# Kernel optimization log

Measured on AMD Instinct MI355X. Metric: run time of the kernel, lower is better.

## Reference

```python
import jax, jax.numpy as jnp
import numpy as np


def setup_inputs() -> dict:
    key = jax.random.key(0)
    k1, k2, k3, k4, k5 = jax.random.split(key, 5)
    N, M, K = 200000, 50, 4
    T = 1000.0
    ti = jnp.sort(jax.random.uniform(k1, (N,), dtype=jnp.float32) * T)
    mi = jax.random.randint(k2, (N,), 0, M, dtype=jnp.int64)
    mu_at_events = jax.random.uniform(k3, (N,), dtype=jnp.float32) * 0.5 + 0.05
    alpha = jax.random.uniform(k4, (K, M, M), dtype=jnp.float32) * 0.1
    gamma = jax.random.uniform(k5, (K,), dtype=jnp.float32) * 2.0 + 0.5
    return {"ti": ti, "mi": mi, "mu_at_events": mu_at_events, "alpha": alpha, "gamma": gamma}


def _hawkes_logsum(ti, mi, mu_at_events, alpha, gamma):
    # ti: [N] sorted event times; mi: [N] event types in [0, M)
    # alpha: [K, M, M]; gamma: [K]; mu_at_events: [N]
    N = ti.shape[0]
    M = alpha.shape[1]
    # inter-event gaps; dt[0] = 0 so the first event has zero excitation state
    dt = jnp.concatenate([jnp.zeros((1,), ti.dtype), ti[1:] - ti[:-1]])  # [N]
    a = jnp.exp(-gamma[None, :] * dt[:, None])  # [N, K] decay factors
    # one-hot of the PREVIOUS event's type (row 0 is all-zero, matching e_mi)
    prev_onehot = jnp.zeros((N, M), ti.dtype).at[jnp.arange(1, N), mi[:-1]].set(1.0)
    b = a[:, None, :] * prev_onehot[:, :, None]  # [N, M, K]

    # linear recurrence S_i = a_i * S_{i-1} + b_i via associative scan
    # combine((a1,b1),(a2,b2)) = (a1*a2, a2*b1 + b2)
    def combine(x, y):
        a1, b1 = x
        a2, b2 = y
        return (a1 * a2, a2[:, None, :] * b1 + b2)

    _, S = jax.lax.associative_scan(combine, (a, b))  # S: [N, M, K]
    # S[i, m, k] = sum_{j < i, m_j = m} exp(-gamma_k (t_i - t_j))
    alpha_at = alpha[:, mi, :]  # [K, N, M] rows of alpha for each event's type
    lam = mu_at_events + jnp.einsum('knm,nmk,k->n', alpha_at, S, gamma)  # [N]
    return jnp.sum(jnp.log(lam))


def reference(ti, mi, mu_at_events, alpha, gamma):
    return _hawkes_logsum(ti, mi, mu_at_events, alpha, gamma)
```

## Files before the change

kernel.cpp:

```cpp
#include <hip/hip_runtime.h>
#include <hip/hip_bf16.h>

#define CHUNK 256
#define MM 50
#define KK 4
#define STATE (MM*KK)
#define ASTRIDE 51
#define SUP 32
#define NSMAX 26

__device__ __forceinline__ unsigned short f2bf(float x) {
  unsigned u = __float_as_uint(x);
  u += 0x7fffu + ((u >> 16) & 1u);
  return (unsigned short)(u >> 16);
}

__global__ __launch_bounds__(256) void phase1(
    const float* __restrict__ ti, const int* __restrict__ mi,
    const float* __restrict__ gamma, float* __restrict__ chunkB,
    float* __restrict__ out0, int N, int G) {
  int g = blockIdx.x, tid = threadIdx.x;
  if (g == 0 && tid == 0) out0[0] = 0.f;
  int l = g * CHUNK;
  int r = min(N, l + CHUNK);
  __shared__ float Bs[STATE];
  __shared__ float g4[KK];
  if (tid < STATE) Bs[tid] = 0.f;
  if (tid < KK) g4[tid] = gamma[tid];
  __syncthreads();
  float t_end = ti[r - 1];
  int j0 = (g == 0) ? 0 : (l - 1);
  int j = j0 + tid;
  if (j <= r - 2) {
    int m = mi[j];
    float dt = t_end - ti[j];
    #pragma unroll
    for (int k = 0; k < KK; ++k)
      atomicAdd(&Bs[m * KK + k], __expf(-g4[k] * dt));
  }
  __syncthreads();
  if (tid < STATE) chunkB[(size_t)g * STATE + tid] = Bs[tid];
}

__global__ __launch_bounds__(256) void phase2a(
    const float* __restrict__ ti, const float* __restrict__ gamma,
    const float* __restrict__ chunkB, float* __restrict__ localpref,
    float* __restrict__ superB, int N, int G) {
  int s = blockIdx.x, tid = threadIdx.x;
  int g0 = s * SUP;
  int gN = min(G, g0 + SUP) - g0;
  __shared__ float te[SUP + 1];
  if (tid <= SUP) {
    int gg = g0 + tid;
    te[tid] = (gg == 0) ? ti[0] : ti[min(N, gg * CHUNK) - 1];
  }
  __syncthreads();
  if (tid >= STATE) return;
  float gk = gamma[tid & 3];
  float B[SUP];
  #pragma unroll
  for (int u = 0; u < SUP; ++u)
    B[u] = (u < gN) ? chunkB[(size_t)(g0 + u) * STATE + tid] : 0.f;
  float S = 0.f;
  #pragma unroll
  for (int u = 0; u < SUP; ++u) {
    if (u < gN) {
      localpref[(size_t)(g0 + u) * STATE + tid] = S;
      if (u == 0) {
        S = B[0];
      } else {
        float a = __expf(-gk * (te[u + 1] - te[u]));
        S = a * S + B[u];
      }
    }
  }
  superB[(size_t)s * STATE + tid] = S;
}

__global__ __launch_bounds__(256) void phase2b(
    const float* __restrict__ ti, const float* __restrict__ gamma,
    const float* __restrict__ superB, float* __restrict__ superpref,
    int N, int nS) {
  int tid = threadIdx.x;
  __shared__ float tlast[NSMAX];
  if (tid < NSMAX)
    tlast[tid] = ti[min(SUP * (tid + 1) * CHUNK, N) - 1];
  __syncthreads();
  if (tid >= STATE) return;
  float gk = gamma[tid & 3];
  float B[NSMAX];
  #pragma unroll
  for (int s = 0; s < NSMAX; ++s)
    B[s] = (s < nS) ? superB[(size_t)s * STATE + tid] : 0.f;
  float S = 0.f;
  superpref[tid] = 0.f;
  #pragma unroll
  for (int s = 0; s < NSMAX; ++s) {
    if (s < nS) {
      if (s == 0) S = B[0];
      else {
        float a = __expf(-gk * (tlast[s] - tlast[s - 1]));
        S = a * S + B[s];
      }
      if (s + 1 < nS) superpref[(size_t)(s + 1) * STATE + tid] = S;
    }
  }
}

__global__ __launch_bounds__(256) void phase3(
    const float* __restrict__ ti, const int* __restrict__ mi,
    const float* __restrict__ mu, const float* __restrict__ alpha,
    const float* __restrict__ gamma, const float* __restrict__ localpref,
    const float* __restrict__ superpref, float* __restrict__ out, int N, int G) {
  int g = blockIdx.x, tid = threadIdx.x;
  int l = g * CHUNK;
  int r = min(N, l + CHUNK);
  int cnt = r - l;
  int sup = g / SUP;

  __shared__ uint2  ALGh[MM * ASTRIDE];
  __shared__ float4 Fj[CHUNK];
  __shared__ int    cj[CHUNK];
  __shared__ float  Q[4][STATE];
  __shared__ float  red[256];

  float gk0 = gamma[0], gk1 = gamma[1], gk2 = gamma[2], gk3 = gamma[3];

  for (int i = tid; i < 4 * STATE; i += 256) ((float*)Q)[i] = 0.f;

  for (int e = tid; e < MM * MM; e += 256) {
    int c = e / MM, cp = e - c * MM;
    float a0 = gk0 * alpha[e];
    float a1 = gk1 * alpha[2500 + e];
    float a2 = gk2 * alpha[5000 + e];
    float a3 = gk3 * alpha[7500 + e];
    ALGh[c * ASTRIDE + cp] =
        make_uint2((unsigned)f2bf(a0) | ((unsigned)f2bf(a1) << 16),
                   (unsigned)f2bf(a2) | ((unsigned)f2bf(a3) << 16));
  }

  int j = l - 1 + tid;
  float t_ref = ti[(g == 0) ? 0 : (l - 1)];
  float4 myF = make_float4(0.f, 0.f, 0.f, 0.f);
  int myc = 0;
  bool valid = (j >= 0) && (j <= r - 2);
  if (valid) {
    myc = mi[j];
    float tj = ti[j] - t_ref;
    myF = make_float4(__expf(gk0 * tj), __expf(gk1 * tj),
                      __expf(gk2 * tj), __expf(gk3 * tj));
  }
  cj[tid] = myc;
  Fj[tid] = myF;
  __syncthreads();

  if (valid) {
    float* q = &Q[tid >> 6][myc * KK];
    atomicAdd(q + 0, myF.x); atomicAdd(q + 1, myF.y);
    atomicAdd(q + 2, myF.z); atomicAdd(q + 3, myF.w);
  }
  __syncthreads();

  if (tid < STATE) {
    float gk = gamma[tid & 3];
    float t_hi = (g > 0) ? ti[(size_t)g * CHUNK - 1] : ti[0];
    float t_lo = (sup > 0) ? ti[(size_t)sup * SUP * CHUNK - 1] : ti[0];
    float D = __expf(-gk * (t_hi - t_lo));
    float sin_v = localpref[(size_t)g * STATE + tid]
                + D * superpref[(size_t)sup * STATE + tid];
    float q0 = Q[0][tid], q1 = Q[1][tid], q2 = Q[2][tid];
    Q[0][tid] = sin_v;
    Q[1][tid] = sin_v + q0;
    Q[2][tid] = sin_v + q0 + q1;
    Q[3][tid] = sin_v + q0 + q1 + q2;
  }
  __syncthreads();

  float local = 0.f;
  if (tid < cnt) {
    int n = l + tid;
    int c_n = mi[n];
    const uint2* arow = &ALGh[c_n * ASTRIDE];
    const float4* wb = (const float4*)&Q[tid >> 6][0];
    float4 acc = make_float4(0.f, 0.f, 0.f, 0.f);
    #pragma unroll 2
    for (int m = 0; m < MM; ++m) {
      uint2 p = arow[m];
      float4 w = wb[m];
      acc.x += __uint_as_float(p.x << 16)          * w.x;
      acc.y += __uint_as_float(p.x & 0xffff0000u)  * w.y;
      acc.z += __uint_as_float(p.y << 16)          * w.z;
      acc.w += __uint_as_float(p.y & 0xffff0000u)  * w.w;
    }
    #pragma unroll 4
    for (int s = (tid & ~63); s <= tid; ++s) {
      uint2 p = arow[cj[s]];
      float4 f = Fj[s];
      acc.x += __uint_as_float(p.x << 16)          * f.x;
      acc.y += __uint_as_float(p.x & 0xffff0000u)  * f.y;
      acc.z += __uint_as_float(p.y << 16)          * f.z;
      acc.w += __uint_as_float(p.y & 0xffff0000u)  * f.w;
    }
    float tn = ti[n] - t_ref;
    float lam = mu[n]
              + __expf(-gk0 * tn) * acc.x + __expf(-gk1 * tn) * acc.y
              + __expf(-gk2 * tn) * acc.z + __expf(-gk3 * tn) * acc.w;
    local = __logf(lam);
  }
  red[tid] = local;
  __syncthreads();
  for (int off = 128; off > 0; off >>= 1) {
    if (tid < off) red[tid] += red[tid + off];
    __syncthreads();
  }
  if (tid == 0) atomicAdd(out, red[0]);
}

extern "C" void kernel_launch(void* const* d_in, const int* in_sizes, int n_in,
                              void* d_out, int out_size, void* d_ws, size_t ws_size,
                              hipStream_t stream) {
  const float* ti    = (const float*)d_in[0];
  const int*   mi    = (const int*)d_in[1];
  const float* mu    = (const float*)d_in[2];
  const float* alpha = (const float*)d_in[3];
  const float* gamma = (const float*)d_in[4];
  float* out = (float*)d_out;
  int N = in_sizes[0];
  int G = (N + CHUNK - 1) / CHUNK;
  int nS = (G + SUP - 1) / SUP;
  float* chunkB    = (float*)d_ws;
  float* localpref = chunkB + (size_t)G * STATE;
  float* superB    = localpref + (size_t)G * STATE;
  float* superpref = superB + (size_t)NSMAX * STATE;

  phase1<<<G, 256, 0, stream>>>(ti, mi, gamma, chunkB, out, N, G);
  phase2a<<<nS, 256, 0, stream>>>(ti, gamma, chunkB, localpref, superB, N, G);
  phase2b<<<1, 256, 0, stream>>>(ti, gamma, superB, superpref, N, nS);
  phase3<<<G, 256, 0, stream>>>(ti, mi, mu, alpha, gamma, localpref, superpref, out, N, G);
}
```

Baseline: 106.1 us.

## Fuse four scan phases into one cooperative kernel with grid syncs

Replaces the four separate launches with a single cooperative kernel that uses grid.sync between the chunk-sum, super-chunk scan, top-level scan and evaluation stages. Chunk sums are now derived from the phase-3 shared-memory partials, so the separate pass over the events is gone. The intra-chunk subgroup size drops from 64 to 32 (8 subgroups), which shortens the per-event quadratic loop. The packed alpha table is split into two 32-bit arrays. The cost is three grid-wide barriers and the constraint that all 782 blocks must be co-resident, which the __launch_bounds__(256,4) hint and the larger shared footprint have to allow.

Result: slower. 328.5 us (+209.5%).

```diff
diff --git a/kernel.cpp b/kernel.cpp
--- a/kernel.cpp
+++ b/kernel.cpp
@@ -1,5 +1,8 @@
 #include <hip/hip_runtime.h>
 #include <hip/hip_bf16.h>
+#include <hip/hip_cooperative_groups.h>
+
+namespace cg = cooperative_groups;
 
 #define CHUNK 256
 #define MM 50
@@ -8,6 +11,8 @@
 #define ASTRIDE 51
 #define SUP 32
 #define NSMAX 26
+#define NSUB 8
+#define SUBSZ 32
 
 __device__ __forceinline__ unsigned short f2bf(float x) {
   unsigned u = __float_as_uint(x);
@@ -15,118 +20,34 @@
   return (unsigned short)(u >> 16);
 }
 
-__global__ __launch_bounds__(256) void phase1(
-    const float* __restrict__ ti, const int* __restrict__ mi,
-    const float* __restrict__ gamma, float* __restrict__ chunkB,
-    float* __restrict__ out0, int N, int G) {
-  int g = blockIdx.x, tid = threadIdx.x;
-  if (g == 0 && tid == 0) out0[0] = 0.f;
-  int l = g * CHUNK;
-  int r = min(N, l + CHUNK);
-  __shared__ float Bs[STATE];
-  __shared__ float g4[KK];
-  if (tid < STATE) Bs[tid] = 0.f;
-  if (tid < KK) g4[tid] = gamma[tid];
-  __syncthreads();
-  float t_end = ti[r - 1];
-  int j0 = (g == 0) ? 0 : (l - 1);
-  int j = j0 + tid;
-  if (j <= r - 2) {
-    int m = mi[j];
-    float dt = t_end - ti[j];
-    #pragma unroll
-    for (int k = 0; k < KK; ++k)
-      atomicAdd(&Bs[m * KK + k], __expf(-g4[k] * dt));
-  }
-  __syncthreads();
-  if (tid < STATE) chunkB[(size_t)g * STATE + tid] = Bs[tid];
-}
-
-__global__ __launch_bounds__(256) void phase2a(
-    const float* __restrict__ ti, const float* __restrict__ gamma,
-    const float* __restrict__ chunkB, float* __restrict__ localpref,
-    float* __restrict__ superB, int N, int G) {
-  int s = blockIdx.x, tid = threadIdx.x;
-  int g0 = s * SUP;
-  int gN = min(G, g0 + SUP) - g0;
-  __shared__ float te[SUP + 1];
-  if (tid <= SUP) {
-    int gg = g0 + tid;
-    te[tid] = (gg == 0) ? ti[0] : ti[min(N, gg * CHUNK) - 1];
-  }
-  __syncthreads();
-  if (tid >= STATE) return;
-  float gk = gamma[tid & 3];
-  float B[SUP];
-  #pragma unroll
-  for (int u = 0; u < SUP; ++u)
-    B[u] = (u < gN) ? chunkB[(size_t)(g0 + u) * STATE + tid] : 0.f;
-  float S = 0.f;
-  #pragma unroll
-  for (int u = 0; u < SUP; ++u) {
-    if (u < gN) {
-      localpref[(size_t)(g0 + u) * STATE + tid] = S;
-      if (u == 0) {
-        S = B[0];
-      } else {
-        float a = __expf(-gk * (te[u + 1] - te[u]));
-        S = a * S + B[u];
-      }
-    }
-  }
-  superB[(size_t)s * STATE + tid] = S;
-}
-
-__global__ __launch_bounds__(256) void phase2b(
-    const float* __restrict__ ti, const float* __restrict__ gamma,
-    const float* __restrict__ superB, float* __restrict__ superpref,
-    int N, int nS) {
-  int tid = threadIdx.x;
-  __shared__ float tlast[NSMAX];
-  if (tid < NSMAX)
-    tlast[tid] = ti[min(SUP * (tid + 1) * CHUNK, N) - 1];
-  __syncthreads();
-  if (tid >= STATE) return;
-  float gk = gamma[tid & 3];
-  float B[NSMAX];
-  #pragma unroll
-  for (int s = 0; s < NSMAX; ++s)
-    B[s] = (s < nS) ? superB[(size_t)s * STATE + tid] : 0.f;
-  float S = 0.f;
-  superpref[tid] = 0.f;
-  #pragma unroll
-  for (int s = 0; s < NSMAX; ++s) {
-    if (s < nS) {
-      if (s == 0) S = B[0];
-      else {
-        float a = __expf(-gk * (tlast[s] - tlast[s - 1]));
-        S = a * S + B[s];
-      }
-      if (s + 1 < nS) superpref[(size_t)(s + 1) * STATE + tid] = S;
-    }
-  }
-}
-
-__global__ __launch_bounds__(256) void phase3(
+__global__ __launch_bounds__(256, 4) void hawkes_all(
     const float* __restrict__ ti, const int* __restrict__ mi,
     const float* __restrict__ mu, const float* __restrict__ alpha,
-    const float* __restrict__ gamma, const float* __restrict__ localpref,
-    const float* __restrict__ superpref, float* __restrict__ out, int N, int G) {
+    const float* __restrict__ gamma,
+    float* __restrict__ chunkB, float* __restrict__ localpref,
+    float* __restrict__ superB, float* __restrict__ superpref,
+    float* __restrict__ out, int N, int G, int nS) {
+  cg::grid_group grid = cg::this_grid();
   int g = blockIdx.x, tid = threadIdx.x;
   int l = g * CHUNK;
   int r = min(N, l + CHUNK);
   int cnt = r - l;
   int sup = g / SUP;
 
-  __shared__ uint2  ALGh[MM * ASTRIDE];
-  __shared__ float4 Fj[CHUNK];
-  __shared__ int    cj[CHUNK];
-  __shared__ float  Q[4][STATE];
-  __shared__ float  red[256];
+  __shared__ unsigned P0[MM * ASTRIDE];
+  __shared__ unsigned P1[MM * ASTRIDE];
+  __shared__ __align__(16) float4 Fj[CHUNK];
+  __shared__ int   cj[CHUNK];
+  __shared__ __align__(16) float Q[NSUB][STATE];
+  __shared__ float red[256];
+  __shared__ float te[SUP + 1];
+  __shared__ float tlast[NSMAX];
+
+  if (g == 0 && tid == 0) out[0] = 0.f;
 
   float gk0 = gamma[0], gk1 = gamma[1], gk2 = gamma[2], gk3 = gamma[3];
 
-  for (int i = tid; i < 4 * STATE; i += 256) ((float*)Q)[i] = 0.f;
+  for (int i = tid; i < NSUB * STATE; i += 256) ((float*)Q)[i] = 0.f;
 
   for (int e = tid; e < MM * MM; e += 256) {
     int c = e / MM, cp = e - c * MM;
@@ -134,9 +55,8 @@
     float a1 = gk1 * alpha[2500 + e];
     float a2 = gk2 * alpha[5000 + e];
     float a3 = gk3 * alpha[7500 + e];
-    ALGh[c * ASTRIDE + cp] =
-        make_uint2((unsigned)f2bf(a0) | ((unsigned)f2bf(a1) << 16),
-                   (unsigned)f2bf(a2) | ((unsigned)f2bf(a3) << 16));
+    P0[c * ASTRIDE + cp] = (unsigned)f2bf(a0) | ((unsigned)f2bf(a1) << 16);
+    P1[c * ASTRIDE + cp] = (unsigned)f2bf(a2) | ((unsigned)f2bf(a3) << 16);
   }
 
   int j = l - 1 + tid;
@@ -155,7 +75,7 @@
   __syncthreads();
 
   if (valid) {
-    float* q = &Q[tid >> 6][myc * KK];
+    float* q = &Q[tid >> 5][myc * KK];
     atomicAdd(q + 0, myF.x); atomicAdd(q + 1, myF.y);
     atomicAdd(q + 2, myF.z); atomicAdd(q + 3, myF.w);
   }
@@ -163,16 +83,88 @@
 
   if (tid < STATE) {
     float gk = gamma[tid & 3];
-    float t_hi = (g > 0) ? ti[(size_t)g * CHUNK - 1] : ti[0];
+    float t_end = ti[r - 1];
+    float Dend = __expf(-gk * (t_end - t_ref));
+    float btot = 0.f;
+    #pragma unroll
+    for (int q = 0; q < NSUB; ++q) btot += Q[q][tid];
+    chunkB[(size_t)g * STATE + tid] = Dend * btot;
+  }
+
+  grid.sync();
+
+  if (g < nS) {
+    int g0 = g * SUP;
+    int gN = min(G, g0 + SUP) - g0;
+    if (tid <= SUP) {
+      int gg = g0 + tid;
+      te[tid] = (gg == 0) ? ti[0] : ti[min(N, gg * CHUNK) - 1];
+    }
+    __syncthreads();
+    if (tid < STATE) {
+      float gk = gamma[tid & 3];
+      float B[SUP];
+      #pragma unroll
+      for (int u = 0; u < SUP; ++u)
+        B[u] = (u < gN) ? chunkB[(size_t)(g0 + u) * STATE + tid] : 0.f;
+      float S = 0.f;
+      #pragma unroll
+      for (int u = 0; u < SUP; ++u) {
+        if (u < gN) {
+          localpref[(size_t)(g0 + u) * STATE + tid] = S;
+          if (u == 0) S = B[0];
+          else {
+            float a = __expf(-gk * (te[u + 1] - te[u]));
+            S = a * S + B[u];
+          }
+        }
+      }
+      superB[(size_t)g * STATE + tid] = S;
+    }
+  }
+
+  grid.sync();
+
+  if (g == 0) {
+    if (tid < NSMAX)
+      tlast[tid] = ti[min(SUP * (tid + 1) * CHUNK, N) - 1];
+    __syncthreads();
+    if (tid < STATE) {
+      float gk = gamma[tid & 3];
+      float B[NSMAX];
+      #pragma unroll
+      for (int s = 0; s < NSMAX; ++s)
+        B[s] = (s < nS) ? superB[(size_t)s * STATE + tid] : 0.f;
+      float S = 0.f;
+      superpref[tid] = 0.f;
+      #pragma unroll
+      for (int s = 0; s < NSMAX; ++s) {
+        if (s < nS) {
+          if (s == 0) S = B[0];
+          else {
+            float a = __expf(-gk * (tlast[s] - tlast[s - 1]));
+            S = a * S + B[s];
+          }
+          if (s + 1 < nS) superpref[(size_t)(s + 1) * STATE + tid] = S;
+        }
+      }
+    }
+  }
+
+  grid.sync();
+
+  if (tid < STATE) {
+    float gk = gamma[tid & 3];
     float t_lo = (sup > 0) ? ti[(size_t)sup * SUP * CHUNK - 1] : ti[0];
-    float D = __expf(-gk * (t_hi - t_lo));
-    float sin_v = localpref[(size_t)g * STATE + tid]
-                + D * superpref[(size_t)sup * STATE + tid];
-    float q0 = Q[0][tid], q1 = Q[1][tid], q2 = Q[2][tid];
-    Q[0][tid] = sin_v;
-    Q[1][tid] = sin_v + q0;
-    Q[2][tid] = sin_v + q0 + q1;
-    Q[3][tid] = sin_v + q0 + q1 + q2;
+    float D = __expf(-gk * (t_ref - t_lo));
+    float run = localpref[(size_t)g * STATE + tid]
+              + D * superpref[(size_t)sup * STATE + tid];
+    #pragma unroll
+    for (int q = 0; q < NSUB; ++q) {
+      float t = Q[q][tid];
+      Q[q][tid] = run;
+      run += t;
+    }
   }
   __syncthreads();
 
@@ -180,26 +172,28 @@
   if (tid < cnt) {
     int n = l + tid;
     int c_n = mi[n];
-    const uint2* arow = &ALGh[c_n * ASTRIDE];
-    const float4* wb = (const float4*)&Q[tid >> 6][0];
+    int rowb = c_n * ASTRIDE;
+    const float4* wb = (const float4*)&Q[tid >> 5][0];
     float4 acc = make_float4(0.f, 0.f, 0.f, 0.f);
     #pragma unroll 2
     for (int m = 0; m < MM; ++m) {
-      uint2 p = arow[m];
+      unsigned p0 = P0[rowb + m];
+      unsigned p1 = P1[rowb + m];
       float4 w = wb[m];
-      acc.x += __uint_as_float(p.x << 16)          * w.x;
-      acc.y += __uint_as_float(p.x & 0xffff0000u)  * w.y;
-      acc.z += __uint_as_float(p.y << 16)          * w.z;
-      acc.w += __uint_as_float(p.y & 0xffff0000u)  * w.w;
+      acc.x += __uint_as_float(p0 << 16)         * w.x;
+      acc.y += __uint_as_float(p0 & 0xffff0000u) * w.y;
+      acc.z += __uint_as_float(p1 << 16)         * w.z;
+      acc.w += __uint_as_float(p1 & 0xffff0000u) * w.w;
     }
     #pragma unroll 4
-    for (int s = (tid & ~63); s <= tid; ++s) {
-      uint2 p = arow[cj[s]];
+    for (int s = (tid & ~(SUBSZ - 1)); s <= tid; ++s) {
+      unsigned p0 = P0[rowb + cj[s]];
+      unsigned p1 = P1[rowb + cj[s]];
       float4 f = Fj[s];
-      acc.x += __uint_as_float(p.x << 16)          * f.x;
-      acc.y += __uint_as_float(p.x & 0xffff0000u)  * f.y;
-      acc.z += __uint_as_float(p.y << 16)          * f.z;
-      acc.w += __uint_as_float(p.y & 0xffff0000u)  * f.w;
+      acc.x += __uint_as_float(p0 << 16)         * f.x;
+      acc.y += __uint_as_float(p0 & 0xffff0000u) * f.y;
+      acc.z += __uint_as_float(p1 << 16)         * f.z;
+      acc.w += __uint_as_float(p1 & 0xffff0000u) * f.w;
     }
     float tn = ti[n] - t_ref;
     float lam = mu[n]
@@ -233,8 +227,8 @@
   float* superB    = localpref + (size_t)G * STATE;
   float* superpref = superB + (size_t)NSMAX * STATE;
 
-  phase1<<<G, 256, 0, stream>>>(ti, mi, gamma, chunkB, out, N, G);
-  phase2a<<<nS, 256, 0, stream>>>(ti, gamma, chunkB, localpref, superB, N, G);
-  phase2b<<<1, 256, 0, stream>>>(ti, gamma, superB, superpref, N, nS);
-  phase3<<<G, 256, 0, stream>>>(ti, mi, mu, alpha, gamma, localpref, superpref, out, N, G);
+  void* args[] = {(void*)&ti, (void*)&mi, (void*)&mu, (void*)&alpha, (void*)&gamma,
+                  (void*)&chunkB, (void*)&localpref, (void*)&superB, (void*)&superpref,
+                  (void*)&out, (void*)&N, (void*)&G, (void*)&nS};
+  hipLaunchCooperativeKernel((void*)hawkes_all, dim3(G), dim3(256), args, 0, stream);
 }
```
